# Kernel optimization log

Measured on AMD Instinct MI355X. Metric: run time of the kernel, lower is better.

## Reference

```python
import jax, jax.numpy as jnp
import numpy as np

B, S, D, N = 4, 1024, 1024, 32768


def setup_inputs() -> dict:
    key = jax.random.key(0)
    ks = jax.random.split(key, 6)
    return {
        "x": jax.random.normal(ks[0], (B, S, D), jnp.float32),
        "h": jax.random.normal(ks[1], (B, S, D), jnp.float32),
        "emb": jax.random.normal(ks[2], (N, D), jnp.float32),
        "tau_offset": jax.random.normal(ks[3], (B, S, 1), jnp.float32) * 0.1,
        "w_read": jax.random.normal(ks[4], (N, D), jnp.float32) * 0.02,
        "w_write": jax.random.normal(ks[5], (N, D), jnp.float32) * 0.02,
        "n_chunks": 8,
    }


def _srw_chunked(x, h, emb_unit, tau_offset, w_read, w_write, n_chunks):
    """Two chunked passes over neuron pool: (1) online score stats, (2) STE
    threshold-gated read->write projection with cost-weighted normalization."""
    Bb, Ss, Dd = x.shape
    Nn = emb_unit.shape[0]
    cs = Nn // n_chunks
    h_bf = h.astype(jnp.bfloat16)
    x_bf = x.astype(jnp.bfloat16)
    emb_bf = emb_unit.astype(jnp.bfloat16)
    read_bf = w_read.astype(jnp.bfloat16)
    write_bf = w_write.astype(jnp.bfloat16)
    z1 = jnp.zeros((Bb, Ss, 1))

    @jax.checkpoint
    def stats_step(carry, i):
        s_sum, sq_sum, ns_sum, ns_sq = carry
        s = i * cs
        ec = jax.lax.dynamic_slice_in_dim(emb_bf, s, cs, axis=0)
        scores = h_bf @ ec.T  # [B,S,cs]
        s_sum = s_sum + scores.sum(axis=-1, keepdims=True).astype(jnp.float32)
        sq_sum = sq_sum + (scores.astype(jnp.float32) ** 2).sum(axis=-1, keepdims=True)
        per_neuron_score = scores.astype(jnp.float32).mean(axis=(0, 1))
        ns_sum = ns_sum + per_neuron_score.sum()
        ns_sq = ns_sq + (per_neuron_score ** 2).sum()
        return ((s_sum, sq_sum, ns_sum, ns_sq), None)

    z_bs1 = jnp.zeros((Bb, Ss, 1))
    z_scalar = jnp.float32(0.0)
    (s_sum, sq_sum, ns_sum, ns_sq), _ = jax.lax.scan(
        stats_step, (z_bs1, z_bs1, z_scalar, z_scalar), jnp.arange(n_chunks))
    s_mean = s_sum / Nn
    s_std = jnp.sqrt(sq_sum / Nn - s_mean ** 2) + 1e-08
    tau = s_mean + tau_offset * s_std
    mean_score = ns_sum / Nn
    var_score = ns_sq / Nn - mean_score ** 2
    score_lb = var_score / (mean_score ** 2 + var_score + 0.01)

    @jax.checkpoint
    def gate_srw_step(carry, i):
        out, total_weighted_cost, total_gate_max, total_active = carry
        s = i * cs
        ec = jax.lax.dynamic_slice_in_dim(emb_bf, s, cs, axis=0)
        rc = jax.lax.dynamic_slice_in_dim(read_bf, s, cs, axis=0)
        wc = jax.lax.dynamic_slice_in_dim(write_bf, s, cs, axis=0)
        rc = rc / (jnp.linalg.norm(rc, axis=-1, keepdims=True) + 1e-08)
        wc = wc / (jnp.linalg.norm(wc, axis=-1, keepdims=True) + 1e-08)
        scores = h_bf @ ec.T
        raw = scores.astype(jnp.float32) - tau
        gate_hard = (raw > 0).astype(jnp.float32)
        sig = jax.nn.sigmoid(raw / s_std)
        gate = gate_hard + sig - jax.lax.stop_gradient(sig)  # straight-through
        gate_bf = gate.astype(jnp.bfloat16)
        xr = x_bf @ rc.T                     # read projection [B,S,cs]
        c_out = (gate_bf * xr @ wc).astype(jnp.float32)  # write projection
        xr_f32 = xr.astype(jnp.float32)
        cost = jax.lax.stop_gradient(xr_f32 ** 2)
        chunk_weighted = (sig * cost).sum(axis=-1, keepdims=True)
        chunk_active = gate_hard.sum(axis=-1, keepdims=True)
        return ((out + c_out,
                 total_weighted_cost + chunk_weighted,
                 jnp.maximum(total_gate_max, gate_hard.max(axis=-1, keepdims=True)),
                 total_active + chunk_active), None)

    (raw_out, total_weighted_cost, total_gate_max, total_active), _ = jax.lax.scan(
        gate_srw_step,
        (jnp.zeros((Bb, Ss, Dd), dtype=jnp.float32), z1,
         jnp.full((Bb, Ss, 1), -1000000000.0), z1),
        jnp.arange(n_chunks))
    den = jnp.sqrt(total_weighted_cost + 1e-06)
    den = jnp.maximum(den, 0.001)
    out = (raw_out / den).astype(jnp.bfloat16)
    score_std_out = s_std.mean()
    es_out = total_weighted_cost.mean()
    active_n_mean = total_active.mean()
    score_mean_out = s_mean.mean()
    return (out.astype(jnp.float32), total_active / Nn, total_gate_max, score_lb,
            score_std_out, es_out, active_n_mean, score_mean_out)


def reference(x, h, emb, tau_offset, w_read, w_write, n_chunks):
    # Caller normalizes the embedding pool to unit rows before the chunked pass.
    emb_unit = emb / (jnp.linalg.norm(emb, axis=-1, keepdims=True) + 1e-08)
    return _srw_chunked(x, h, emb_unit, tau_offset, w_read, w_write, n_chunks)
```

## Files before the change

kernel.cpp:

```cpp
#include <hip/hip_runtime.h>
#include <stdint.h>

#define M_TOT 4096
#define D_DIM 1024
#define N_NEUR 32768
#define NCHUNK 8
#define CS 4096

typedef float f32x4 __attribute__((ext_vector_type(4)));
typedef __bf16 bf16x8 __attribute__((ext_vector_type(8)));
typedef unsigned short u16;
typedef unsigned int u32;
typedef u16 u16x8 __attribute__((ext_vector_type(8)));
typedef u16 u16x4 __attribute__((ext_vector_type(4)));

__device__ __forceinline__ u16 f2bf(float f) {
    u32 u = __builtin_bit_cast(u32, f);
    u = (u + 0x7FFFu + ((u >> 16) & 1u)) >> 16;
    return (u16)u;
}
__device__ __forceinline__ float bf2f(u16 h) {
    u32 u = ((u32)h) << 16;
    return __builtin_bit_cast(float, u);
}
__device__ __forceinline__ u32 pack2(float a, float b, float s) {
    return (u32)f2bf(a * s) | ((u32)f2bf(b * s) << 16);
}

typedef __attribute__((address_space(1))) const u32 as1_u32;
typedef __attribute__((address_space(3))) u32 as3_u32;
__device__ __forceinline__ void gload16(const void* g, void* l) {
    __builtin_amdgcn_global_load_lds((as1_u32*)g, (as3_u32*)l, 16, 0, 0);
}

#define MFMA(a, b, c) __builtin_amdgcn_mfma_f32_16x16x32_bf16((a), (b), (c), 0, 0, 0)

#define GEMM128_BODY(ABASE, ASTR, BBASE, BSTR, KLEN)                                  \
    __shared__ u16 LDS[17408];                                                        \
    u16* Al = LDS;                                                                    \
    u16* Bl = LDS + 4096;                                                             \
    const int t = threadIdx.x, lane = t & 63, w = t >> 6;                             \
    const int wr = w >> 1, wc = w & 1, l15 = lane & 15, lg = lane >> 4;               \
    f32x4 acc[4][4] = {};                                                             \
    {                                                                                 \
        const int rb = lane >> 2, cl = (lane & 3) * 8;                                \
        const int seg0 = w * 2;                                                       \
        const size_t ro0 = (size_t)(seg0 * 16 + rb);                                  \
        const u16* pa0 = (ABASE) + ((size_t)bm * 128 + ro0) * (ASTR) + cl;            \
        const u16* pb0 = (BBASE) + ((size_t)bn * 128 + ro0) * (BSTR) + cl;            \
        const u16* pa1 = pa0 + (size_t)16 * (ASTR);                                   \
        const u16* pb1 = pb0 + (size_t)16 * (BSTR);                                   \
        u16* la0 = Al + seg0 * 512;                                                   \
        u16* lb0 = Bl + seg0 * 512;                                                   \
        for (int k0 = 0; k0 < (KLEN); k0 += 32) {                                     \
            __syncthreads();                                                          \
            gload16(pa0 + k0, la0);                                                   \
            gload16(pa1 + k0, la0 + 512);                                             \
            gload16(pb0 + k0, lb0);                                                   \
            gload16(pb1 + k0, lb0 + 512);                                             \
            __syncthreads();                                                          \
            bf16x8 afr[4], bfr[4];                                                    \
            _Pragma("unroll") for (int m = 0; m < 4; m++)                             \
                afr[m] = *(const bf16x8*)&Al[(wr * 64 + m * 16 + l15) * 32 + lg * 8]; \
            _Pragma("unroll") for (int n = 0; n < 4; n++)                             \
                bfr[n] = *(const bf16x8*)&Bl[(wc * 64 + n * 16 + l15) * 32 + lg * 8]; \
            _Pragma("unroll") for (int m = 0; m < 4; m++)                             \
                _Pragma("unroll") for (int n = 0; n < 4; n++)                         \
                    acc[m][n] = MFMA(afr[m], bfr[n], acc[m][n]);                      \
        }                                                                             \
    }

#define RESTAGE_TO_LDS(VALS)                                                          \
    __syncthreads();                                                                  \
    _Pragma("unroll") for (int m = 0; m < 4; m++)                                     \
        _Pragma("unroll") for (int rr = 0; rr < 4; rr++)                              \
            _Pragma("unroll") for (int n = 0; n < 4; n++) {                           \
                int lrow = wr * 64 + m * 16 + lg * 4 + rr;                            \
                LDS[lrow * 136 + wc * 64 + n * 16 + l15] = (VALS);                    \
            }                                                                         \
    __syncthreads();

#define RESTAGE_U16_TILE(VALS, DSTBASE, DSTSTRIDE, COLBASE)                           \
    {                                                                                 \
        RESTAGE_TO_LDS(VALS)                                                          \
        int row_ = t >> 2, c0_ = (t & 3) * 32;                                        \
        _Pragma("unroll") for (int p = 0; p < 2; p++) {                               \
            int lrow = p * 64 + row_;                                                 \
            u16* dst_ = (DSTBASE) + (size_t)(bm * 128 + lrow) * (DSTSTRIDE) +         \
                        (COLBASE) + c0_;                                              \
            const u16* srcl_ = &LDS[lrow * 136 + c0_];                                \
            _Pragma("unroll") for (int j = 0; j < 4; j++)                             \
                *(u16x8*)(dst_ + j * 8) = *(const u16x8*)(srcl_ + j * 8);             \
        }                                                                             \
    }

__global__ __launch_bounds__(256) void k_cvt(const float* __restrict__ h,
                                             const float* __restrict__ x,
                                             u16* __restrict__ hb, u16* __restrict__ xb) {
    size_t i = ((size_t)blockIdx.x * 256 + threadIdx.x) * 4;
    float4 v = *(const float4*)(h + i);
    uint2 o;
    o.x = pack2(v.x, v.y, 1.0f);
    o.y = pack2(v.z, v.w, 1.0f);
    *(uint2*)(hb + i) = o;
    v = *(const float4*)(x + i);
    o.x = pack2(v.x, v.y, 1.0f);
    o.y = pack2(v.z, v.w, 1.0f);
    *(uint2*)(xb + i) = o;
}

__global__ __launch_bounds__(256) void k_cvt_ern(const float* __restrict__ emb,
                                                 const float* __restrict__ wrd,
                                                 u16* __restrict__ ebf, u16* __restrict__ rbf) {
    int t = threadIdx.x, lane = t & 63, wv = t >> 6;
    int row = blockIdx.x * 4 + wv;
    bool isE = blockIdx.y == 0;
    const float4* src = (const float4*)((isE ? emb : wrd) + (size_t)row * D_DIM);
    float4 v[4];
    float ss = 0.f;
#pragma unroll
    for (int j = 0; j < 4; j++) {
        v[j] = src[j * 64 + lane];
        if (isE) {
            ss += v[j].x * v[j].x + v[j].y * v[j].y + v[j].z * v[j].z + v[j].w * v[j].w;
        } else {
            float a = bf2f(f2bf(v[j].x)), b = bf2f(f2bf(v[j].y));
            float c = bf2f(f2bf(v[j].z)), d = bf2f(f2bf(v[j].w));
            ss += a * a + b * b + c * c + d * d;
        }
    }
#pragma unroll
    for (int s = 1; s < 64; s <<= 1) ss += __shfl_xor(ss, s);
    float sc = 1.0f / (sqrtf(ss) + 1e-8f);
    uint2* dst = (uint2*)((isE ? ebf : rbf) + (size_t)row * D_DIM);
#pragma unroll
    for (int j = 0; j < 4; j++) {
        uint2 o;
        o.x = pack2(v[j].x, v[j].y, sc);
        o.y = pack2(v[j].z, v[j].w, sc);
        dst[j * 64 + lane] = o;
    }
}

__global__ __launch_bounds__(256) void k_cvt_e_norm(const float* __restrict__ emb,
                                                    int cbase, u16* __restrict__ ebf) {
    int t = threadIdx.x, lane = t & 63, wv = t >> 6;
    int row = blockIdx.x * 4 + wv;
    const float4* src = (const float4*)(emb + (size_t)(cbase + row) * D_DIM);
    float4 v[4];
    float ss = 0.f;
#pragma unroll
    for (int j = 0; j < 4; j++) {
        v[j] = src[j * 64 + lane];
        ss += v[j].x * v[j].x + v[j].y * v[j].y + v[j].z * v[j].z + v[j].w * v[j].w;
    }
#pragma unroll
    for (int s = 1; s < 64; s <<= 1) ss += __shfl_xor(ss, s);
    float es = 1.0f / (sqrtf(ss) + 1e-8f);
    uint2* dst = (uint2*)(ebf + (size_t)row * D_DIM);
#pragma unroll
    for (int j = 0; j < 4; j++) {
        uint2 o;
        o.x = pack2(v[j].x, v[j].y, es);
        o.y = pack2(v[j].z, v[j].w, es);
        dst[j * 64 + lane] = o;
    }
}

__global__ __launch_bounds__(256) void k_cvt_r_norm(const float* __restrict__ wrd,
                                                    int cbase, u16* __restrict__ rbf) {
    int t = threadIdx.x, lane = t & 63, wv = t >> 6;
    int row = blockIdx.x * 4 + wv;
    const float4* src = (const float4*)(wrd + (size_t)(cbase + row) * D_DIM);
    float4 v[4];
    float ss = 0.f;
#pragma unroll
    for (int j = 0; j < 4; j++) {
        v[j] = src[j * 64 + lane];
        float a = bf2f(f2bf(v[j].x)), b = bf2f(f2bf(v[j].y));
        float c = bf2f(f2bf(v[j].z)), d = bf2f(f2bf(v[j].w));
        ss += a * a + b * b + c * c + d * d;
    }
#pragma unroll
    for (int s = 1; s < 64; s <<= 1) ss += __shfl_xor(ss, s);
    float rs = 1.0f / (sqrtf(ss) + 1e-8f);
    uint2* dst = (uint2*)(rbf + (size_t)row * D_DIM);
#pragma unroll
    for (int j = 0; j < 4; j++) {
        uint2 o;
        o.x = pack2(v[j].x, v[j].y, rs);
        o.y = pack2(v[j].z, v[j].w, rs);
        dst[j * 64 + lane] = o;
    }
}

__global__ __launch_bounds__(256) void k_sw(const float* __restrict__ ww, float* sw) {
    int t = threadIdx.x, lane = t & 63, wv = t >> 6;
    int row = blockIdx.x * 4 + wv;
    const float4* src = (const float4*)(ww + (size_t)row * D_DIM);
    float ss = 0.f;
#pragma unroll
    for (int j = 0; j < 4; j++) {
        float4 v = src[j * 64 + lane];
        float a = bf2f(f2bf(v.x)), b = bf2f(f2bf(v.y));
        float c = bf2f(f2bf(v.z)), d = bf2f(f2bf(v.w));
        ss += a * a + b * b + c * c + d * d;
    }
#pragma unroll
    for (int s = 1; s < 64; s <<= 1) ss += __shfl_xor(ss, s);
    if (lane == 0) sw[row] = 1.0f / (sqrtf(ss) + 1e-8f);
}

__global__ __launch_bounds__(256) void k_tww(const float* __restrict__ ww,
                                             const float* __restrict__ sw,
                                             int cbase, u16* __restrict__ wwT, int dstr) {
    __shared__ u16 tile[64][80];
    int kt = blockIdx.x * 64;
    int dt = blockIdx.y * 64;
    int t = threadIdx.x;
    int kk = t >> 4;
    int dd = (t & 15) * 4;
#pragma unroll
    for (int i = 0; i < 4; i++) {
        int krow = kk + i * 16;
        int kg = cbase + kt + krow;
        float s = sw[kg];
        float4 v = *(const float4*)(ww + (size_t)kg * D_DIM + dt + dd);
        tile[dd + 0][krow] = f2bf(v.x * s);
        tile[dd + 1][krow] = f2bf(v.y * s);
        tile[dd + 2][krow] = f2bf(v.z * s);
        tile[dd + 3][krow] = f2bf(v.w * s);
    }
    __syncthreads();
    int dd2 = t >> 2;
    int kk2 = (t & 3) * 16;
    uint4 o0 = *(const uint4*)&tile[dd2][kk2];
    uint4 o1 = *(const uint4*)&tile[dd2][kk2 + 8];
    u16* dst = wwT + (size_t)(dt + dd2) * dstr + kt + kk2;
    *(uint4*)dst = o0;
    *(uint4*)(dst + 8) = o1;
}

__global__ __launch_bounds__(256) void k_pass1(const u16* __restrict__ hb,
                                               const u16* __restrict__ ebf, int cbase,
                                               float* rowsum, float* rowsq, float* colsum,
                                               u16* __restrict__ sb, int sstr) {
    int bm = blockIdx.x, bn = blockIdx.y;
    GEMM128_BODY(hb, D_DIM, ebf, D_DIM, D_DIM)
    float csv[4] = {0.f, 0.f, 0.f, 0.f};
#pragma unroll
    for (int m = 0; m < 4; m++)
#pragma unroll
        for (int rr = 0; rr < 4; rr++)
#pragma unroll
            for (int n = 0; n < 4; n++) csv[n] += bf2f(f2bf(acc[m][n][rr]));
#pragma unroll
    for (int n = 0; n < 4; n++) {
        float cv = csv[n];
        cv += __shfl_xor(cv, 16);
        cv += __shfl_xor(cv, 32);
        if (lg == 0) {
            int ng = cbase + bn * 128 + wc * 64 + n * 16 + l15;
            atomicAdd(&colsum[ng], cv);
        }
    }
    RESTAGE_TO_LDS(f2bf(acc[m][n][rr]))
    int row_ = t >> 2, c0_ = (t & 3) * 32;
#pragma unroll
    for (int p = 0; p < 2; p++) {
        int lrow = p * 64 + row_;
        int grow = bm * 128 + lrow;
        float rs = 0.f, rq = 0.f;
        u16* dst = sb ? (sb + (size_t)grow * sstr + cbase + bn * 128 + c0_) : (u16*)nullptr;
#pragma unroll
        for (int j = 0; j < 4; j++) {
            u16x8 v = *(const u16x8*)&LDS[lrow * 136 + c0_ + j * 8];
            if (dst) *(u16x8*)(dst + j * 8) = v;
#pragma unroll
            for (int q = 0; q < 8; q++) {
                float sv = bf2f(v[q]);
                rs += sv;
                rq += sv * sv;
            }
        }
        rs += __shfl_xor(rs, 1);
        rq += __shfl_xor(rq, 1);
        rs += __shfl_xor(rs, 2);
        rq += __shfl_xor(rq, 2);
        if ((lane & 3) == 0) {
            atomicAdd(&rowsum[grow], rs);
            atomicAdd(&rowsq[grow], rq);
        }
    }
}

__global__ __launch_bounds__(256) void k_ns(const float* __restrict__ colsum, float* scal) {
    int i = blockIdx.x * 256 + threadIdx.x;
    float pm = colsum[i] * (1.0f / 4096.0f);
    float s1 = pm, s2 = pm * pm;
#pragma unroll
    for (int x = 1; x < 64; x <<= 1) {
        s1 += __shfl_xor(s1, x);
        s2 += __shfl_xor(s2, x);
    }
    __shared__ float sh[2][4];
    int w = threadIdx.x >> 6;
    if ((threadIdx.x & 63) == 0) { sh[0][w] = s1; sh[1][w] = s2; }
    __syncthreads();
    if (threadIdx.x == 0) {
        atomicAdd(&scal[0], sh[0][0] + sh[0][1] + sh[0][2] + sh[0][3]);
        atomicAdd(&scal[1], sh[1][0] + sh[1][1] + sh[1][2] + sh[1][3]);
    }
}

__global__ __launch_bounds__(256) void k_tau(const float* __restrict__ rowsum,
                                             const float* __restrict__ rowsq,
                                             const float* __restrict__ tau_off,
                                             float* tau, float* invstd, float* smean, float* sstd) {
    int i = blockIdx.x * 256 + threadIdx.x;
    float sm = rowsum[i] * (1.0f / 32768.0f);
    float var = rowsq[i] * (1.0f / 32768.0f) - sm * sm;
    float sd = sqrtf(var) + 1e-8f;
    smean[i] = sm;
    sstd[i] = sd;
    invstd[i] = 1.0f / sd;
    tau[i] = sm + tau_off[i] * sd;
}

__global__ __launch_bounds__(256) void k_xr_gate_all(const u16* __restrict__ xb,
                                                     const u16* __restrict__ rbf,
                                                     u16* __restrict__ sbP,
                                                     const float* __restrict__ tau,
                                                     const float* __restrict__ invstd,
                                                     float* twc, float* act) {
    int bm = blockIdx.x, bn = blockIdx.y;
    const int tt = threadIdx.x;
    const int prow = tt >> 2, pc0 = (tt & 3) * 32;
    u16x8 sv_pre[2][4];
#pragma unroll
    for (int p = 0; p < 2; p++) {
        int grow = bm * 128 + p * 64 + prow;
        const u16* src = sbP + (size_t)grow * N_NEUR + bn * 128 + pc0;
#pragma unroll
        for (int j = 0; j < 4; j++) sv_pre[p][j] = *(const u16x8*)(src + j * 8);
    }
    GEMM128_BODY(xb, D_DIM, rbf, D_DIM, D_DIM)
    RESTAGE_TO_LDS(f2bf(acc[m][n][rr]))
#pragma unroll
    for (int p = 0; p < 2; p++) {
        int lrow = p * 64 + prow;
        int grow = bm * 128 + lrow;
        float tl = tau[grow], il = invstd[grow];
        float wsum = 0.f, cnt = 0.f;
        u16* gptr = sbP + (size_t)grow * N_NEUR + bn * 128 + pc0;
#pragma unroll
        for (int j = 0; j < 4; j++) {
            u16x8 xr8 = *(const u16x8*)&LDS[lrow * 136 + pc0 + j * 8];
            u16x8 sv8 = sv_pre[p][j];
            u16x8 o;
#pragma unroll
            for (int q = 0; q < 8; q++) {
                float xf = bf2f(xr8[q]);
                float raw = bf2f(sv8[q]) - tl;
                float sig = 1.0f / (1.0f + __expf(-raw * il));
                bool g = raw > 0.0f;
                wsum += sig * xf * xf;
                cnt += g ? 1.0f : 0.0f;
                o[q] = g ? xr8[q] : (u16)0;
            }
            *(u16x8*)(gptr + j * 8) = o;
        }
        wsum += __shfl_xor(wsum, 1);
        cnt += __shfl_xor(cnt, 1);
        wsum += __shfl_xor(wsum, 2);
        cnt += __shfl_xor(cnt, 2);
        if ((lane & 3) == 0) {
            atomicAdd(&twc[grow], wsum);
            atomicAdd(&act[grow], cnt);
        }
    }
}

__global__ __launch_bounds__(256) void k_pass2b_all(const u16* __restrict__ sbP,
                                                    const u16* __restrict__ wwT,
                                                    u16* __restrict__ part) {
    int bm = blockIdx.x;
    int bn = blockIdx.y;
    int zz = blockIdx.z;
    const u16* Pz = sbP + (size_t)zz * CS;
    const u16* Wz = wwT + (size_t)zz * CS;
    u16* pz = part + (size_t)zz * M_TOT * D_DIM;
    GEMM128_BODY(Pz, N_NEUR, Wz, N_NEUR, CS)
    RESTAGE_U16_TILE(f2bf(acc[m][n][rr]), pz, D_DIM, bn * 128)
}

__global__ __launch_bounds__(256) void k_norm_comb(const u16* __restrict__ part,
                                                   const float* __restrict__ twc,
                                                   const float* __restrict__ act,
                                                   float* __restrict__ out0,
                                                   float* out1, float* out2) {
    int row = blockIdx.x;
    float den = sqrtf(twc[row] + 1e-6f);
    den = fmaxf(den, 0.001f);
    float inv = 1.0f / den;
    size_t base = (size_t)row * D_DIM + threadIdx.x * 4;
    float s0 = 0.f, s1 = 0.f, s2 = 0.f, s3 = 0.f;
#pragma unroll
    for (int c = 0; c < NCHUNK; c++) {
        u16x4 v = *(const u16x4*)(part + (size_t)c * M_TOT * D_DIM + base);
        s0 += bf2f(v[0]);
        s1 += bf2f(v[1]);
        s2 += bf2f(v[2]);
        s3 += bf2f(v[3]);
    }
    float4 o;
    o.x = bf2f(f2bf(s0 * inv));
    o.y = bf2f(f2bf(s1 * inv));
    o.z = bf2f(f2bf(s2 * inv));
    o.w = bf2f(f2bf(s3 * inv));
    *(float4*)(out0 + base) = o;
    if (threadIdx.x == 0) {
        out1[row] = act[row] * (1.0f / 32768.0f);
        out2[row] = act[row] > 0.0f ? 1.0f : 0.0f;
    }
}

__global__ __launch_bounds__(256) void k_xr_plain(const u16* __restrict__ xb,
                                                  const u16* __restrict__ rbf,
                                                  u16* __restrict__ P) {
    int bm = blockIdx.x, bn = blockIdx.y;
    GEMM128_BODY(xb, D_DIM, rbf, D_DIM, D_DIM)
    RESTAGE_U16_TILE(f2bf(acc[m][n][rr]), P, CS, bn * 128)
}

__global__ __launch_bounds__(256) void k_gate_gemm(const u16* __restrict__ hb,
                                                   const u16* __restrict__ ebf,
                                                   const float* __restrict__ tau,
                                                   const float* __restrict__ invstd,
                                                   u16* __restrict__ P, float* twc, float* act) {
    int bm = blockIdx.x, bn = blockIdx.y;
    GEMM128_BODY(hb, D_DIM, ebf, D_DIM, D_DIM)
#pragma unroll
    for (int m = 0; m < 4; m++) {
#pragma unroll
        for (int rr = 0; rr < 4; rr++) {
            int mg = bm * 128 + wr * 64 + m * 16 + lg * 4 + rr;
            float tl = tau[mg], il = invstd[mg];
            float wsum = 0.f, cnt = 0.f;
#pragma unroll
            for (int n = 0; n < 4; n++) {
                int ngl = bn * 128 + wc * 64 + n * 16 + l15;
                float sv = bf2f(f2bf(acc[m][n][rr]));
                float raw = sv - tl;
                u16 xrb = P[(size_t)mg * CS + ngl];
                float xf = bf2f(xrb);
                float sig = 1.0f / (1.0f + __expf(-raw * il));
                bool g = raw > 0.0f;
                wsum += sig * xf * xf;
                cnt += g ? 1.0f : 0.0f;
                P[(size_t)mg * CS + ngl] = g ? xrb : (u16)0;
            }
#pragma unroll
            for (int x = 1; x < 16; x <<= 1) {
                wsum += __shfl_xor(wsum, x);
                cnt += __shfl_xor(cnt, x);
            }
            if (l15 == 0) {
                atomicAdd(&twc[mg], wsum);
                atomicAdd(&act[mg], cnt);
            }
        }
    }
}

__global__ __launch_bounds__(256) void k_pass2b(const u16* __restrict__ P,
                                                const u16* __restrict__ wwT, int bstr,
                                                float* __restrict__ out) {
    int bm = blockIdx.x;
    int bn = blockIdx.y;
    GEMM128_BODY(P, CS, wwT, bstr, CS)
#pragma unroll
    for (int m = 0; m < 4; m++)
#pragma unroll
        for (int n = 0; n < 4; n++)
#pragma unroll
            for (int rr = 0; rr < 4; rr++) {
                int mg = bm * 128 + wr * 64 + m * 16 + lg * 4 + rr;
                int dg = bn * 128 + wc * 64 + n * 16 + l15;
                out[(size_t)mg * D_DIM + dg] += bf2f(f2bf(acc[m][n][rr]));
            }
}

__global__ __launch_bounds__(256) void k_norm_f(float* __restrict__ out,
                                                const float* __restrict__ twc,
                                                const float* __restrict__ act,
                                                float* out1, float* out2) {
    int row = blockIdx.x;
    float den = sqrtf(twc[row] + 1e-6f);
    den = fmaxf(den, 0.001f);
    float inv = 1.0f / den;
    float* p = out + (size_t)row * D_DIM;
    int i = threadIdx.x * 4;
    float4 v = *(float4*)(p + i);
    v.x = bf2f(f2bf(v.x * inv));
    v.y = bf2f(f2bf(v.y * inv));
    v.z = bf2f(f2bf(v.z * inv));
    v.w = bf2f(f2bf(v.w * inv));
    *(float4*)(p + i) = v;
    if (threadIdx.x == 0) {
        out1[row] = act[row] * (1.0f / 32768.0f);
        out2[row] = act[row] > 0.0f ? 1.0f : 0.0f;
    }
}

__global__ __launch_bounds__(256) void k_scalars(const float* __restrict__ smean,
                                                 const float* __restrict__ sstd,
                                                 const float* __restrict__ twc,
                                                 const float* __restrict__ act,
                                                 const float* __restrict__ scal,
                                                 float* outS) {
    float a = 0.f, b = 0.f, c = 0.f, d = 0.f;
    for (int i = threadIdx.x; i < 4096; i += 256) {
        a += smean[i];
        b += sstd[i];
        c += twc[i];
        d += act[i];
    }
#pragma unroll
    for (int x = 1; x < 64; x <<= 1) {
        a += __shfl_xor(a, x);
        b += __shfl_xor(b, x);
        c += __shfl_xor(c, x);
        d += __shfl_xor(d, x);
    }
    __shared__ float sh[4][4];
    int w = threadIdx.x >> 6;
    if ((threadIdx.x & 63) == 0) { sh[0][w] = a; sh[1][w] = b; sh[2][w] = c; sh[3][w] = d; }
    __syncthreads();
    if (threadIdx.x == 0) {
        float ma = sh[0][0] + sh[0][1] + sh[0][2] + sh[0][3];
        float mb = sh[1][0] + sh[1][1] + sh[1][2] + sh[1][3];
        float mc = sh[2][0] + sh[2][1] + sh[2][2] + sh[2][3];
        float md = sh[3][0] + sh[3][1] + sh[3][2] + sh[3][3];
        float mean_score = scal[0] * (1.0f / 32768.0f);
        float var_score = scal[1] * (1.0f / 32768.0f) - mean_score * mean_score;
        outS[0] = var_score / (mean_score * mean_score + var_score + 0.01f);
        outS[1] = mb * (1.0f / 4096.0f);
        outS[2] = mc * (1.0f / 4096.0f);
        outS[3] = md * (1.0f / 4096.0f);
        outS[4] = ma * (1.0f / 4096.0f);
    }
}

static constexpr size_t OFF_HB     = 0;
static constexpr size_t OFF_XB     = 8388608;
static constexpr size_t OFF_P      = 16777216;
static constexpr size_t OFF_EBF    = 50331648;
static constexpr size_t OFF_RBF    = 117440512;
static constexpr size_t OFF_WWT    = 184549376;
static constexpr size_t OFF_SW     = 251658240;
static constexpr size_t OFF_ROWSUM = 251789312;
static constexpr size_t OFF_ROWSQ  = 251805696;
static constexpr size_t OFF_COLSUM = 251822080;
static constexpr size_t OFF_TAU    = 251953152;
static constexpr size_t OFF_INVSTD = 251969536;
static constexpr size_t OFF_SMEAN  = 251985920;
static constexpr size_t OFF_SSTD   = 252002304;
static constexpr size_t OFF_TWC    = 252018688;
static constexpr size_t OFF_ACT    = 252035072;
static constexpr size_t OFF_SCAL   = 252051456;
static constexpr size_t STATS_END  = 252051520;
static constexpr size_t ZERO_LEN   = STATS_END - OFF_ROWSUM;
static constexpr size_t OFF_SB     = 252706816;
static constexpr size_t FULL_END   = OFF_SB + (size_t)M_TOT * N_NEUR * 2;
static constexpr size_t OFF_PART   = OFF_EBF;

extern "C" void kernel_launch(void* const* d_in, const int* in_sizes, int n_in,
                              void* d_out, int out_size, void* d_ws, size_t ws_size,
                              hipStream_t stream) {
    const float* x = (const float*)d_in[0];
    const float* h = (const float*)d_in[1];
    const float* emb = (const float*)d_in[2];
    const float* tau_off = (const float*)d_in[3];
    const float* w_read = (const float*)d_in[4];
    const float* w_write = (const float*)d_in[5];
    char* ws = (char*)d_ws;
    u16* hb = (u16*)(ws + OFF_HB);
    u16* xb = (u16*)(ws + OFF_XB);
    u16* P = (u16*)(ws + OFF_P);
    u16* ebf = (u16*)(ws + OFF_EBF);
    u16* rbf = (u16*)(ws + OFF_RBF);
    u16* wwT = (u16*)(ws + OFF_WWT);
    float* sw = (float*)(ws + OFF_SW);
    float* rowsum = (float*)(ws + OFF_ROWSUM);
    float* rowsq = (float*)(ws + OFF_ROWSQ);
    float* colsum = (float*)(ws + OFF_COLSUM);
    float* tau = (float*)(ws + OFF_TAU);
    float* invstd = (float*)(ws + OFF_INVSTD);
    float* smean = (float*)(ws + OFF_SMEAN);
    float* sstd = (float*)(ws + OFF_SSTD);
    float* twc = (float*)(ws + OFF_TWC);
    float* act = (float*)(ws + OFF_ACT);
    float* scal = (float*)(ws + OFF_SCAL);
    u16* part = (u16*)(ws + OFF_PART);
    const bool fullA = ws_size >= FULL_END;
    u16* sbP = fullA ? (u16*)(ws + OFF_SB) : (u16*)nullptr;

    float* out0 = (float*)d_out;
    float* out1 = out0 + (size_t)M_TOT * D_DIM;
    float* out2 = out1 + M_TOT;
    float* outS = out2 + M_TOT;

    hipMemsetAsync(ws + OFF_ROWSUM, 0, ZERO_LEN, stream);

    k_cvt<<<4096, 256, 0, stream>>>(h, x, hb, xb);
    k_sw<<<N_NEUR / 4, 256, 0, stream>>>(w_write, sw);

    if (fullA) {
        k_cvt_ern<<<dim3(N_NEUR / 4, 2), 256, 0, stream>>>(emb, w_read, ebf, rbf);
        k_tww<<<dim3(N_NEUR / 64, 16), 256, 0, stream>>>(w_write, sw, 0, wwT, N_NEUR);
        k_pass1<<<dim3(32, 256), 256, 0, stream>>>(hb, ebf, 0, rowsum, rowsq, colsum,
                                                   sbP, N_NEUR);
        k_ns<<<128, 256, 0, stream>>>(colsum, scal);
        k_tau<<<16, 256, 0, stream>>>(rowsum, rowsq, tau_off, tau, invstd, smean, sstd);
        k_xr_gate_all<<<dim3(32, 256), 256, 0, stream>>>(xb, rbf, sbP, tau, invstd, twc, act);
        k_pass2b_all<<<dim3(32, 8, 8), 256, 0, stream>>>(sbP, wwT, part);
        k_norm_comb<<<4096, 256, 0, stream>>>(part, twc, act, out0, out1, out2);
    } else {
        hipMemsetAsync(d_out, 0, (size_t)M_TOT * D_DIM * 4, stream);
        for (int c = 0; c < NCHUNK; c++) {
            k_cvt_e_norm<<<CS / 4, 256, 0, stream>>>(emb, c * CS, ebf);
            k_pass1<<<dim3(32, 32), 256, 0, stream>>>(hb, ebf, c * CS, rowsum, rowsq, colsum,
                                                      (u16*)nullptr, 0);
        }
        k_ns<<<128, 256, 0, stream>>>(colsum, scal);
        k_tau<<<16, 256, 0, stream>>>(rowsum, rowsq, tau_off, tau, invstd, smean, sstd);
        for (int c = 0; c < NCHUNK; c++) {
            k_cvt_e_norm<<<CS / 4, 256, 0, stream>>>(emb, c * CS, ebf);
            k_cvt_r_norm<<<CS / 4, 256, 0, stream>>>(w_read, c * CS, rbf);
            k_tww<<<dim3(CS / 64, 16), 256, 0, stream>>>(w_write, sw, c * CS, wwT, CS);
            k_xr_plain<<<dim3(32, 32), 256, 0, stream>>>(xb, rbf, P);
            k_gate_gemm<<<dim3(32, 32), 256, 0, stream>>>(hb, ebf, tau, invstd, P, twc, act);
            k_pass2b<<<dim3(32, 8), 256, 0, stream>>>(P, wwT, CS, out0);
        }
        k_norm_f<<<4096, 256, 0, stream>>>(out0, twc, act, out1, out2);
    }
    k_scalars<<<1, 256, 0, stream>>>(smean, sstd, twc, act, scal, outS);
}
```

Baseline: 1.527 ms.

## Double GEMM K-step to 64 and fold write-norm kernel into conversion launch

The shared GEMM body now stages a 128x64 K-slab per iteration instead of 128x32. Each wave issues eight 16-byte global-to-LDS loads, and the MFMA loop runs two K sub-steps between barriers, which halves the number of __syncthreads pairs per GEMM. Separately, the w_write row-norm kernel is merged into the emb/w_read conversion launch as a third grid slice, saving one launch in the full-workspace path. The 64-element row stride in LDS may raise bank conflicts on fragment reads, and the larger tile uses more LDS.

```diff
diff --git a/kernel.cpp b/kernel.cpp
--- a/kernel.cpp
+++ b/kernel.cpp
@@ -38,35 +38,36 @@
 #define GEMM128_BODY(ABASE, ASTR, BBASE, BSTR, KLEN)                                  \
     __shared__ u16 LDS[17408];                                                        \
     u16* Al = LDS;                                                                    \
-    u16* Bl = LDS + 4096;                                                             \
+    u16* Bl = LDS + 8192;                                                             \
     const int t = threadIdx.x, lane = t & 63, w = t >> 6;                             \
     const int wr = w >> 1, wc = w & 1, l15 = lane & 15, lg = lane >> 4;               \
     f32x4 acc[4][4] = {};                                                             \
     {                                                                                 \
-        const int rb = lane >> 2, cl = (lane & 3) * 8;                                \
-        const int seg0 = w * 2;                                                       \
-        const size_t ro0 = (size_t)(seg0 * 16 + rb);                                  \
-        const u16* pa0 = (ABASE) + ((size_t)bm * 128 + ro0) * (ASTR) + cl;            \
-        const u16* pb0 = (BBASE) + ((size_t)bn * 128 + ro0) * (BSTR) + cl;            \
-        const u16* pa1 = pa0 + (size_t)16 * (ASTR);                                   \
-        const u16* pb1 = pb0 + (size_t)16 * (BSTR);                                   \
-        u16* la0 = Al + seg0 * 512;                                                   \
-        u16* lb0 = Bl + seg0 * 512;                                                   \
-        for (int k0 = 0; k0 < (KLEN); k0 += 32) {                                     \
+        const int srow = w * 8 + (lane >> 3);                                         \
+        const int scol = (lane & 7) * 8;                                              \
+        const u16* pa = (ABASE) + ((size_t)bm * 128 + srow) * (ASTR) + scol;          \
+        const u16* pb = (BBASE) + ((size_t)bn * 128 + srow) * (BSTR) + scol;          \
+        u16* lda = Al + w * 512;                                                      \
+        u16* ldb = Bl + w * 512;                                                      \
+        for (int k0 = 0; k0 < (KLEN); k0 += 64) {                                     \
             __syncthreads();                                                          \
-            gload16(pa0 + k0, la0);                                                   \
-            gload16(pa1 + k0, la0 + 512);                                             \
-            gload16(pb0 + k0, lb0);                                                   \
-            gload16(pb1 + k0, lb0 + 512);                                             \
+            _Pragma("unroll") for (int r = 0; r < 4; r++) {                           \
+                gload16(pa + (size_t)(r * 32) * (ASTR) + k0, lda + r * 2048);         \
+                gload16(pb + (size_t)(r * 32) * (BSTR) + k0, ldb + r * 2048);         \
+            }                                                                         \
             __syncthreads();                                                          \
-            bf16x8 afr[4], bfr[4];                                                    \
-            _Pragma("unroll") for (int m = 0; m < 4; m++)                             \
-                afr[m] = *(const bf16x8*)&Al[(wr * 64 + m * 16 + l15) * 32 + lg * 8]; \
-            _Pragma("unroll") for (int n = 0; n < 4; n++)                             \
-                bfr[n] = *(const bf16x8*)&Bl[(wc * 64 + n * 16 + l15) * 32 + lg * 8]; \
-            _Pragma("unroll") for (int m = 0; m < 4; m++)                             \
+            _Pragma("unroll") for (int ks = 0; ks < 2; ks++) {                        \
+                bf16x8 afr[4], bfr[4];                                                \
+                _Pragma("unroll") for (int m = 0; m < 4; m++)                         \
+                    afr[m] = *(const bf16x8*)&Al[(wr * 64 + m * 16 + l15) * 64 +      \
+                                                 ks * 32 + lg * 8];                   \
                 _Pragma("unroll") for (int n = 0; n < 4; n++)                         \
-                    acc[m][n] = MFMA(afr[m], bfr[n], acc[m][n]);                      \
+                    bfr[n] = *(const bf16x8*)&Bl[(wc * 64 + n * 16 + l15) * 64 +      \
+                                                 ks * 32 + lg * 8];                   \
+                _Pragma("unroll") for (int m = 0; m < 4; m++)                         \
+                    _Pragma("unroll") for (int n = 0; n < 4; n++)                     \
+                        acc[m][n] = MFMA(afr[m], bfr[n], acc[m][n]);                  \
+            }                                                                         \
         }                                                                             \
     }
 
@@ -109,19 +110,22 @@
     *(uint2*)(xb + i) = o;
 }
 
-__global__ __launch_bounds__(256) void k_cvt_ern(const float* __restrict__ emb,
-                                                 const float* __restrict__ wrd,
-                                                 u16* __restrict__ ebf, u16* __restrict__ rbf) {
+__global__ __launch_bounds__(256) void k_cvt_ern3(const float* __restrict__ emb,
+                                                  const float* __restrict__ wrd,
+                                                  const float* __restrict__ ww,
+                                                  u16* __restrict__ ebf, u16* __restrict__ rbf,
+                                                  float* __restrict__ sw) {
     int t = threadIdx.x, lane = t & 63, wv = t >> 6;
     int row = blockIdx.x * 4 + wv;
-    bool isE = blockIdx.y == 0;
-    const float4* src = (const float4*)((isE ? emb : wrd) + (size_t)row * D_DIM);
+    int which = blockIdx.y;
+    const float* srcm = which == 0 ? emb : (which == 1 ? wrd : ww);
+    const float4* src = (const float4*)(srcm + (size_t)row * D_DIM);
     float4 v[4];
     float ss = 0.f;
 #pragma unroll
     for (int j = 0; j < 4; j++) {
         v[j] = src[j * 64 + lane];
-        if (isE) {
+        if (which == 0) {
             ss += v[j].x * v[j].x + v[j].y * v[j].y + v[j].z * v[j].z + v[j].w * v[j].w;
         } else {
             float a = bf2f(f2bf(v[j].x)), b = bf2f(f2bf(v[j].y));
@@ -132,7 +136,11 @@
 #pragma unroll
     for (int s = 1; s < 64; s <<= 1) ss += __shfl_xor(ss, s);
     float sc = 1.0f / (sqrtf(ss) + 1e-8f);
-    uint2* dst = (uint2*)((isE ? ebf : rbf) + (size_t)row * D_DIM);
+    if (which == 2) {
+        if (lane == 0) sw[row] = sc;
+        return;
+    }
+    uint2* dst = (uint2*)((which == 0 ? ebf : rbf) + (size_t)row * D_DIM);
 #pragma unroll
     for (int j = 0; j < 4; j++) {
         uint2 o;
@@ -614,10 +622,10 @@
     hipMemsetAsync(ws + OFF_ROWSUM, 0, ZERO_LEN, stream);
 
     k_cvt<<<4096, 256, 0, stream>>>(h, x, hb, xb);
-    k_sw<<<N_NEUR / 4, 256, 0, stream>>>(w_write, sw);
 
     if (fullA) {
-        k_cvt_ern<<<dim3(N_NEUR / 4, 2), 256, 0, stream>>>(emb, w_read, ebf, rbf);
+        k_cvt_ern3<<<dim3(N_NEUR / 4, 3), 256, 0, stream>>>(emb, w_read, w_write,
+                                                            ebf, rbf, sw);
         k_tww<<<dim3(N_NEUR / 64, 16), 256, 0, stream>>>(w_write, sw, 0, wwT, N_NEUR);
         k_pass1<<<dim3(32, 256), 256, 0, stream>>>(hb, ebf, 0, rowsum, rowsq, colsum,
                                                    sbP, N_NEUR);
@@ -628,6 +636,7 @@
         k_norm_comb<<<4096, 256, 0, stream>>>(part, twc, act, out0, out1, out2);
     } else {
         hipMemsetAsync(d_out, 0, (size_t)M_TOT * D_DIM * 4, stream);
+        k_sw<<<N_NEUR / 4, 256, 0, stream>>>(w_write, sw);
         for (int c = 0; c < NCHUNK; c++) {
             k_cvt_e_norm<<<CS / 4, 256, 0, stream>>>(emb, c * CS, ebf);
             k_pass1<<<dim3(32, 32), 256, 0, stream>>>(hb, ebf, c * CS, rowsum, rowsq, colsum,
```

New measurement: 1.648 ms. +7.9%, slower.
